# Optimization experiments

Measured on AMD Instinct MI355X. Metric: run time of the kernel, lower is better.

The kernel has to match this reference:

```python
import jax, jax.numpy as jnp
import numpy as np

B, LP, LQ, H = 16, 512, 512, 768


def setup_inputs() -> dict:
    key = jax.random.key(0)
    k0, k1, k2, k3 = jax.random.split(key, 4)
    proj_p = jax.random.normal(k0, (B, LP, H), dtype=jnp.float32)
    proj_q = jax.random.normal(k1, (B, LQ, H), dtype=jnp.float32)
    seq_len = jax.random.randint(k2, (B,), 1, LQ + 1)  # valid lengths in [1, LQ]
    W_trans = jax.random.normal(k3, (H, H), dtype=jnp.float32) / jnp.sqrt(H).astype(jnp.float32)
    b_trans = jnp.zeros((H,), dtype=jnp.float32)
    return {"proj_p": proj_p, "proj_q": proj_q, "seq_len": seq_len,
            "W_trans": W_trans, "b_trans": b_trans}


def reference(proj_p, proj_q, seq_len, W_trans, b_trans):
    # trans_q = trans_linear(proj_q): [B, Lq, H]
    trans_q = jnp.einsum('bqh,oh->bqo', proj_q, W_trans) + b_trans
    # attention scores: [B, Lp, Lq]
    att = jnp.einsum('bph,bqh->bpq', proj_p, trans_q)
    # masked_softmax (MedLane style): softmax(scores * mask), re-mask, renormalize
    mask = (jnp.arange(LQ)[None, None, :] < seq_len[:, None, None]).astype(att.dtype)
    probs = jax.nn.softmax(att * mask, axis=-1) * mask
    probs = probs / (jnp.sum(probs, axis=-1, keepdims=True) + 1e-13)
    # weighted sum of proj_q: [B, Lp, H]
    att_vec = jnp.einsum('bpq,bqh->bph', probs, proj_q)
    # output = ReLU(trans_linear(att_vec))
    out = jax.nn.relu(jnp.einsum('bph,oh->bpo', att_vec, W_trans) + b_trans)
    return out
```

## Files before the change

kernel.cpp:

```cpp
#include <hip/hip_runtime.h>

typedef _Float16 f16x8 __attribute__((ext_vector_type(8)));
typedef __attribute__((ext_vector_type(4))) float f32x4;
typedef unsigned short u16;

__device__ __forceinline__ u16 f2h(float f) {
    _Float16 h = (_Float16)f;
    return __builtin_bit_cast(u16, h);
}

#define GLDS(G, LBYTE)                                                         \
    __builtin_amdgcn_global_load_lds(                                          \
        (const __attribute__((address_space(1))) void*)(G),                    \
        (__attribute__((address_space(3))) void*)((char*)lds + (LBYTE)),       \
        16, 0, 0)

template<int OUT, bool BIAS, bool RELU, bool RS, int GX, int GY>
__global__ __launch_bounds__(256, 3)
void gemm_nt(const u16* __restrict__ A, const u16* __restrict__ B,
             const float* __restrict__ bias, const float* __restrict__ rs,
             void* __restrict__ Cv,
             int K, int lda, int ldb, int ldc,
             long sA, long sB, long sC)
{
    __shared__ u16 lds[24576];
    constexpr int BOF  = 8192;
    constexpr int BUFB = 24576;
    constexpr int BUFE = 12288;

    const unsigned flat = blockIdx.x;
    const unsigned cpx  = gridDim.x >> 3;
    const unsigned id   = (flat & 7u) * cpx + (flat >> 3);
    const int bz  = (int)(id / (unsigned)(GX * GY));
    const int rem = (int)(id - (unsigned)bz * (GX * GY));
    const int by  = rem / GX;
    const int bx  = rem - by * GX;

    const int tid  = threadIdx.x;
    const int lane = tid & 63;
    const int wid  = tid >> 6;
    const int m0 = by * 128;
    const int n0 = bx * 64;

    const int rowS = tid >> 3;
    const int sl   = (tid & 7) ^ (rowS & 7);
    const unsigned ldsW = (unsigned)wid * 1024u;

    const u16* aS = A + (size_t)bz * sA + ((size_t)m0 + rowS) * lda + sl * 8;
    const u16* bS = B + (size_t)bz * sB + ((size_t)n0 + rowS) * ldb + sl * 8;

    const int wm = (wid & 1) * 64;
    const int wn = (wid >> 1) * 32;
    const int fr = lane & 15;
    const int fq = lane >> 4;

    f32x4 acc[4][2] = {};

    auto stage = [&](int bb, int k0) {
        GLDS(aS + k0,            bb +     0 + ldsW);
        GLDS(aS + k0 + 32 * lda, bb +  4096 + ldsW);
        GLDS(aS + k0 + 64 * lda, bb +  8192 + ldsW);
        GLDS(aS + k0 + 96 * lda, bb + 12288 + ldsW);
        GLDS(bS + k0,            bb + 16384 + ldsW);
        GLDS(bS + k0 + 32 * ldb, bb + 20480 + ldsW);
    };

    auto compute = [&](int be) {
#pragma unroll
        for (int w = 0; w < 2; ++w) {
            const int sw = (((w << 2) | fq) ^ (fr & 7)) << 3;
            f16x8 vah[4], vbh[2];
#pragma unroll
            for (int i = 0; i < 4; ++i)
                vah[i] = *(const f16x8*)(lds + be + (wm + i * 16 + fr) * 64 + sw);
#pragma unroll
            for (int j = 0; j < 2; ++j)
                vbh[j] = *(const f16x8*)(lds + be + BOF + (wn + j * 16 + fr) * 64 + sw);
#pragma unroll
            for (int i = 0; i < 4; ++i)
#pragma unroll
                for (int j = 0; j < 2; ++j)
                    acc[i][j] = __builtin_amdgcn_mfma_f32_16x16x32_f16(vah[i], vbh[j], acc[i][j], 0, 0, 0);
        }
    };

    stage(0, 0);
    __syncthreads();
    for (int k0 = 0; k0 < K; k0 += 128) {
        if (k0 + 64 < K) stage(BUFB, k0 + 64);
        compute(0);
        __syncthreads();
        if (k0 + 128 < K) stage(0, k0 + 128);
        compute(BUFE);
        __syncthreads();
    }

    float bj[2];
    if (BIAS) {
#pragma unroll
        for (int j = 0; j < 2; ++j) bj[j] = bias[n0 + wn + j * 16 + fr];
    }
    const long crow0 = m0 + wm + fq * 4;
    const long ccol0 = n0 + wn + fr;
    float* Cf = (float*)Cv + (size_t)bz * sC;
    u16*   Ch = (u16*)Cv   + (size_t)bz * sC;
    const float* rsb = RS ? (rs + (size_t)bz * 512) : nullptr;
#pragma unroll
    for (int i = 0; i < 4; ++i) {
        float rsv[4];
        if (RS) {
#pragma unroll
            for (int r = 0; r < 4; ++r) rsv[r] = 1.0f - rsb[crow0 + i * 16 + r];
        }
#pragma unroll
        for (int j = 0; j < 2; ++j)
#pragma unroll
            for (int r = 0; r < 4; ++r) {
                float v = acc[i][j][r];
                if (BIAS) v += RS ? bj[j] * rsv[r] : bj[j];
                if (RELU) v = fmaxf(v, 0.0f);
                const size_t idx = (size_t)(crow0 + i * 16 + r) * ldc + ccol0 + j * 16;
                if (OUT == 0) Cf[idx] = v;
                else          Ch[idx] = f2h(v);
            }
    }
}

__global__ __launch_bounds__(256)
void cvt2_f32_f16(const float* __restrict__ x0, u16* __restrict__ y0,
                  const float* __restrict__ x1, u16* __restrict__ y1, int n4)
{
    int i = blockIdx.x * 256 + threadIdx.x;
    const int stride = gridDim.x * 256;
    for (; i < n4; i += stride) {
        float4 v0 = ((const float4*)x0)[i];
        float4 v1 = ((const float4*)x1)[i];
        ushort4 h0, h1;
        h0.x = f2h(v0.x); h0.y = f2h(v0.y); h0.z = f2h(v0.z); h0.w = f2h(v0.w);
        h1.x = f2h(v1.x); h1.y = f2h(v1.y); h1.z = f2h(v1.z); h1.w = f2h(v1.w);
        ((ushort4*)y0)[i] = h0;
        ((ushort4*)y1)[i] = h1;
    }
}

__global__ __launch_bounds__(256)
void cvt_f32_f16(const float* __restrict__ x, u16* __restrict__ y, int n4)
{
    int i = blockIdx.x * 256 + threadIdx.x;
    const int stride = gridDim.x * 256;
    for (; i < n4; i += stride) {
        float4 v = ((const float4*)x)[i];
        ushort4 h;
        h.x = f2h(v.x); h.y = f2h(v.y); h.z = f2h(v.z); h.w = f2h(v.w);
        ((ushort4*)y)[i] = h;
    }
}

__global__ __launch_bounds__(256)
void transpose_f16(const u16* __restrict__ src, u16* __restrict__ dst)
{
    __shared__ u16 t[32][33];
    const int z = blockIdx.z;
    src += (size_t)z * 512 * 768;
    dst += (size_t)z * 768 * 512;
    const int h0 = blockIdx.x * 32;
    const int q0 = blockIdx.y * 32;
    const int tx = threadIdx.x;
    const int ty = threadIdx.y;
#pragma unroll
    for (int r = 0; r < 4; ++r)
        t[ty * 4 + r][tx] = src[(size_t)(q0 + ty * 4 + r) * 768 + h0 + tx];
    __syncthreads();
#pragma unroll
    for (int r = 0; r < 4; ++r)
        dst[(size_t)(h0 + ty * 4 + r) * 512 + q0 + tx] = t[tx][ty * 4 + r];
}

__global__ __launch_bounds__(256)
void softmax_kernel(float* __restrict__ att, const int* __restrict__ seq_len,
                    float* __restrict__ rsout)
{
    const int row = blockIdx.x;
    const int b   = row >> 9;
    float* s = att + (size_t)row * 512;
    const int L = seq_len[b];
    const int tid = threadIdx.x;

    __shared__ float red[4];

    const float v0 = s[tid];
    const float v1 = s[tid + 256];
    const float s0 = (tid < L) ? v0 : 0.0f;
    const float s1 = (tid + 256 < L) ? v1 : 0.0f;

    float m = fmaxf(s0, s1);
#pragma unroll
    for (int o = 32; o > 0; o >>= 1) m = fmaxf(m, __shfl_down(m, o));
    if ((tid & 63) == 0) red[tid >> 6] = m;
    __syncthreads();
    const float M = fmaxf(fmaxf(red[0], red[1]), fmaxf(red[2], red[3]));
    __syncthreads();

    const float e0 = expf(s0 - M);
    const float e1 = expf(s1 - M);

    float zs = e0 + e1;
#pragma unroll
    for (int o = 32; o > 0; o >>= 1) zs += __shfl_down(zs, o);
    if ((tid & 63) == 0) red[tid >> 6] = zs;
    __syncthreads();
    const float Z = red[0] + red[1] + red[2] + red[3];
    __syncthreads();

    const float p0 = (tid < L)       ? e0 / Z : 0.0f;
    const float p1 = (tid + 256 < L) ? e1 / Z : 0.0f;

    float ss = p0 + p1;
#pragma unroll
    for (int o = 32; o > 0; o >>= 1) ss += __shfl_down(ss, o);
    if ((tid & 63) == 0) red[tid >> 6] = ss;
    __syncthreads();
    const float S = red[0] + red[1] + red[2] + red[3];

    const float inv = 1.0f / (S + 1e-13f);
    u16* o16 = (u16*)s;
    o16[tid]       = f2h(p0 * inv);
    o16[tid + 256] = f2h(p1 * inv);
    if (tid == 0) rsout[row] = S * inv;
}

extern "C" void kernel_launch(void* const* d_in, const int* in_sizes, int n_in,
                              void* d_out, int out_size, void* d_ws, size_t ws_size,
                              hipStream_t stream)
{
    (void)in_sizes; (void)n_in; (void)out_size; (void)ws_size;
    constexpr int B = 16, L = 512, H = 768;
    constexpr size_t NPQ = (size_t)B * L * H;
    constexpr size_t NW  = (size_t)H * H;

    const float* proj_p  = (const float*)d_in[0];
    const float* proj_q  = (const float*)d_in[1];
    const int*   seq_len = (const int*)d_in[2];
    const float* W       = (const float*)d_in[3];
    const float* bias    = (const float*)d_in[4];
    float* out = (float*)d_out;

    u16* ws   = (u16*)d_ws;
    u16* pq16 = ws;
    u16* pp16 = pq16 + NPQ;
    u16* W16  = pp16 + NPQ;
    u16* tqT  = W16 + NW;
    float* att = (float*)(tqT + NPQ);
    float* rs  = att + (size_t)B * L * L;

    u16* tq16 = (u16*)d_out;

    cvt_f32_f16<<<576, 256, 0, stream>>>(W, W16, (int)(NW / 4));
    cvt2_f32_f16<<<2048, 256, 0, stream>>>(proj_q, pq16, proj_p, pp16, (int)(NPQ / 4));

    gemm_nt<1, true, false, false, 12, 64><<<768, 256, 0, stream>>>(
        pq16, W16, bias, nullptr, tq16, H, H, H, H, 0, 0, 0);

    transpose_f16<<<dim3(24, 16, 16), dim3(32, 8), 0, stream>>>(tq16, tqT);

    gemm_nt<0, false, false, false, 8, 4><<<512, 256, 0, stream>>>(
        pp16, tq16, nullptr, nullptr, att, H, H, H, L,
        (long)L * H, (long)L * H, (long)L * L);

    softmax_kernel<<<B * L, 256, 0, stream>>>(att, seq_len, rs);

    gemm_nt<0, true, true, true, 12, 4><<<768, 256, 0, stream>>>(
        (const u16*)att, tqT, bias, rs, out,
        L, 1024, L, H, (long)L * 1024, (long)H * L, (long)L * H);
}
```

Before: 80.31 us.

## Fuse transpose into first GEMM epilogue, merge conversions, simplify softmax reductions

Measured after the change: 71.47 us. 11.0% less time.

```diff
diff --git a/kernel.cpp b/kernel.cpp
--- a/kernel.cpp
+++ b/kernel.cpp
@@ -15,11 +15,11 @@
         (__attribute__((address_space(3))) void*)((char*)lds + (LBYTE)),       \
         16, 0, 0)
 
-template<int OUT, bool BIAS, bool RELU, bool RS, int GX, int GY>
+template<int OUT, bool BIAS, bool RELU, bool RS, bool TW, int GX, int GY>
 __global__ __launch_bounds__(256, 3)
 void gemm_nt(const u16* __restrict__ A, const u16* __restrict__ B,
              const float* __restrict__ bias, const float* __restrict__ rs,
-             void* __restrict__ Cv,
+             void* __restrict__ Cv, u16* __restrict__ CT,
              int K, int lda, int ldb, int ldc,
              long sA, long sB, long sC)
 {
@@ -105,6 +105,8 @@
     float* Cf = (float*)Cv + (size_t)bz * sC;
     u16*   Ch = (u16*)Cv   + (size_t)bz * sC;
     const float* rsb = RS ? (rs + (size_t)bz * 512) : nullptr;
+    const int  bzT = (int)(crow0 >> 9);
+    const long qb  = crow0 & 511;
 #pragma unroll
     for (int i = 0; i < 4; ++i) {
         float rsv[4];
@@ -113,7 +115,8 @@
             for (int r = 0; r < 4; ++r) rsv[r] = 1.0f - rsb[crow0 + i * 16 + r];
         }
 #pragma unroll
-        for (int j = 0; j < 2; ++j)
+        for (int j = 0; j < 2; ++j) {
+            ushort4 tw;
 #pragma unroll
             for (int r = 0; r < 4; ++r) {
                 float v = acc[i][j][r];
@@ -121,14 +124,24 @@
                 if (RELU) v = fmaxf(v, 0.0f);
                 const size_t idx = (size_t)(crow0 + i * 16 + r) * ldc + ccol0 + j * 16;
                 if (OUT == 0) Cf[idx] = v;
-                else          Ch[idx] = f2h(v);
+                else {
+                    const u16 h = f2h(v);
+                    Ch[idx] = h;
+                    if (TW) (&tw.x)[r] = h;
+                }
             }
+            if (OUT == 1 && TW) {
+                *(ushort4*)(CT + (size_t)bzT * 768 * 512
+                               + (size_t)(ccol0 + j * 16) * 512 + qb + i * 16) = tw;
+            }
+        }
     }
 }
 
 __global__ __launch_bounds__(256)
-void cvt2_f32_f16(const float* __restrict__ x0, u16* __restrict__ y0,
-                  const float* __restrict__ x1, u16* __restrict__ y1, int n4)
+void cvt_all(const float* __restrict__ x0, u16* __restrict__ y0,
+             const float* __restrict__ x1, u16* __restrict__ y1, int n4,
+             const float* __restrict__ xw, u16* __restrict__ yw, int nW4)
 {
     int i = blockIdx.x * 256 + threadIdx.x;
     const int stride = gridDim.x * 256;
@@ -140,40 +153,13 @@
         h1.x = f2h(v1.x); h1.y = f2h(v1.y); h1.z = f2h(v1.z); h1.w = f2h(v1.w);
         ((ushort4*)y0)[i] = h0;
         ((ushort4*)y1)[i] = h1;
-    }
-}
-
-__global__ __launch_bounds__(256)
-void cvt_f32_f16(const float* __restrict__ x, u16* __restrict__ y, int n4)
-{
-    int i = blockIdx.x * 256 + threadIdx.x;
-    const int stride = gridDim.x * 256;
-    for (; i < n4; i += stride) {
-        float4 v = ((const float4*)x)[i];
-        ushort4 h;
-        h.x = f2h(v.x); h.y = f2h(v.y); h.z = f2h(v.z); h.w = f2h(v.w);
-        ((ushort4*)y)[i] = h;
-    }
-}
-
-__global__ __launch_bounds__(256)
-void transpose_f16(const u16* __restrict__ src, u16* __restrict__ dst)
-{
-    __shared__ u16 t[32][33];
-    const int z = blockIdx.z;
-    src += (size_t)z * 512 * 768;
-    dst += (size_t)z * 768 * 512;
-    const int h0 = blockIdx.x * 32;
-    const int q0 = blockIdx.y * 32;
-    const int tx = threadIdx.x;
-    const int ty = threadIdx.y;
-#pragma unroll
-    for (int r = 0; r < 4; ++r)
-        t[ty * 4 + r][tx] = src[(size_t)(q0 + ty * 4 + r) * 768 + h0 + tx];
-    __syncthreads();
-#pragma unroll
-    for (int r = 0; r < 4; ++r)
-        dst[(size_t)(h0 + ty * 4 + r) * 512 + q0 + tx] = t[tx][ty * 4 + r];
+        if (i < nW4) {
+            float4 vw = ((const float4*)xw)[i];
+            ushort4 hw;
+            hw.x = f2h(vw.x); hw.y = f2h(vw.y); hw.z = f2h(vw.z); hw.w = f2h(vw.w);
+            ((ushort4*)yw)[i] = hw;
+        }
+    }
 }
 
 __global__ __launch_bounds__(256)
@@ -190,8 +176,10 @@
 
     const float v0 = s[tid];
     const float v1 = s[tid + 256];
-    const float s0 = (tid < L) ? v0 : 0.0f;
-    const float s1 = (tid + 256 < L) ? v1 : 0.0f;
+    const bool  k0 = (tid < L);
+    const bool  k1 = (tid + 256 < L);
+    const float s0 = k0 ? v0 : 0.0f;
+    const float s1 = k1 ? v1 : 0.0f;
 
     float m = fmaxf(s0, s1);
 #pragma unroll
@@ -201,31 +189,24 @@
     const float M = fmaxf(fmaxf(red[0], red[1]), fmaxf(red[2], red[3]));
     __syncthreads();
 
-    const float e0 = expf(s0 - M);
-    const float e1 = expf(s1 - M);
+    const float e0 = k0 ? expf(s0 - M) : 0.0f;
+    const float e1 = k1 ? expf(s1 - M) : 0.0f;
 
     float zs = e0 + e1;
 #pragma unroll
     for (int o = 32; o > 0; o >>= 1) zs += __shfl_down(zs, o);
     if ((tid & 63) == 0) red[tid >> 6] = zs;
     __syncthreads();
-    const float Z = red[0] + red[1] + red[2] + red[3];
-    __syncthreads();
-
-    const float p0 = (tid < L)       ? e0 / Z : 0.0f;
-    const float p1 = (tid + 256 < L) ? e1 / Z : 0.0f;
-
-    float ss = p0 + p1;
-#pragma unroll
-    for (int o = 32; o > 0; o >>= 1) ss += __shfl_down(ss, o);
-    if ((tid & 63) == 0) red[tid >> 6] = ss;
-    __syncthreads();
-    const float S = red[0] + red[1] + red[2] + red[3];
-
+    const float sve = red[0] + red[1] + red[2] + red[3];
+
+    const float Z   = sve + (float)(512 - L) * expf(-M);
+    const float S   = sve / Z;
     const float inv = 1.0f / (S + 1e-13f);
+    const float sc  = inv / Z;
+
     u16* o16 = (u16*)s;
-    o16[tid]       = f2h(p0 * inv);
-    o16[tid + 256] = f2h(p1 * inv);
+    o16[tid]       = f2h(k0 ? e0 * sc : 0.0f);
+    o16[tid + 256] = f2h(k1 ? e1 * sc : 0.0f);
     if (tid == 0) rsout[row] = S * inv;
 }
 
@@ -255,21 +236,19 @@
 
     u16* tq16 = (u16*)d_out;
 
-    cvt_f32_f16<<<576, 256, 0, stream>>>(W, W16, (int)(NW / 4));
-    cvt2_f32_f16<<<2048, 256, 0, stream>>>(proj_q, pq16, proj_p, pp16, (int)(NPQ / 4));
-
-    gemm_nt<1, true, false, false, 12, 64><<<768, 256, 0, stream>>>(
-        pq16, W16, bias, nullptr, tq16, H, H, H, H, 0, 0, 0);
-
-    transpose_f16<<<dim3(24, 16, 16), dim3(32, 8), 0, stream>>>(tq16, tqT);
-
-    gemm_nt<0, false, false, false, 8, 4><<<512, 256, 0, stream>>>(
-        pp16, tq16, nullptr, nullptr, att, H, H, H, L,
+    cvt_all<<<2048, 256, 0, stream>>>(proj_q, pq16, proj_p, pp16, (int)(NPQ / 4),
+                                      W, W16, (int)(NW / 4));
+
+    gemm_nt<1, true, false, false, true, 12, 64><<<768, 256, 0, stream>>>(
+        pq16, W16, bias, nullptr, tq16, tqT, H, H, H, H, 0, 0, 0);
+
+    gemm_nt<0, false, false, false, false, 8, 4><<<512, 256, 0, stream>>>(
+        pp16, tq16, nullptr, nullptr, att, nullptr, H, H, H, L,
         (long)L * H, (long)L * H, (long)L * L);
 
     softmax_kernel<<<B * L, 256, 0, stream>>>(att, seq_len, rs);
 
-    gemm_nt<0, true, true, true, 12, 4><<<768, 256, 0, stream>>>(
-        (const u16*)att, tqT, bias, rs, out,
+    gemm_nt<0, true, true, true, false, 12, 4><<<768, 256, 0, stream>>>(
+        (const u16*)att, tqT, bias, rs, out, nullptr,
         L, 1024, L, H, (long)L * 1024, (long)H * L, (long)L * H);
 }
```
